# Kernel tuning notes

Measured on AMD Instinct MI355X. Metric: run time of the kernel, lower is better.

## Reference

```python
import jax, jax.numpy as jnp
import numpy as np

N = 100_000      # nodes
E = 3_200_000    # edges
F_IN = 9
F_HID = 9
F_OUT = 1
EPS = 1e-5

def _ln(x, g, b):
    m = x.mean(-1, keepdims=True)
    v = x.var(-1, keepdims=True)
    return (x - m) / jnp.sqrt(v + EPS) * g + b

def _gat(x, src, dst, edge_attr, W, a_src, a_dst, We, a_e, bias):
    # Single-head GATConv with edge_dim=1, add_self_loops=True, fill_value='mean'
    n = x.shape[0]
    loop = jnp.arange(n)
    deg = jax.ops.segment_sum(jnp.ones((src.shape[0],), x.dtype), dst, n)
    loop_attr = jax.ops.segment_sum(edge_attr, dst, n) / jnp.maximum(deg, 1.0)[:, None]
    s = jnp.concatenate([src, loop])
    d = jnp.concatenate([dst, loop])
    ea = jnp.concatenate([edge_attr, loop_attr], axis=0)   # [E+N, 1]
    xp = x @ W                                             # [N, C]
    a = (xp * a_src).sum(-1)[s] + (xp * a_dst).sum(-1)[d] + ((ea @ We) * a_e).sum(-1)
    a = jax.nn.leaky_relu(a, 0.2)
    amax = jax.ops.segment_max(a, d, n)
    aexp = jnp.exp(a - amax[d])
    denom = jax.ops.segment_sum(aexp, d, n)
    alpha = aexp / (denom[d] + 1e-16)
    return jax.ops.segment_sum(alpha[:, None] * xp[s], d, n) + bias

def setup_inputs() -> dict:
    key = jax.random.key(0)
    ks = jax.random.split(key, 16)
    def rn(k, shp, s):
        return jax.random.normal(k, shp, jnp.float32) * s
    return {
        "x": jax.random.normal(ks[0], (N, F_IN), jnp.float32),
        "edge_index": jax.random.randint(ks[1], (2, E), 0, N, jnp.int32),
        "edge_attr": jax.random.normal(ks[2], (E, 1), jnp.float32),
        "ln1_g": jnp.ones((F_IN,), jnp.float32), "ln1_b": jnp.zeros((F_IN,), jnp.float32),
        "W0": rn(ks[3], (F_IN, F_HID), 0.3), "as0": rn(ks[4], (F_HID,), 0.3),
        "ad0": rn(ks[5], (F_HID,), 0.3), "We0": rn(ks[6], (1, F_HID), 0.3),
        "ae0": rn(ks[7], (F_HID,), 0.3), "b0": jnp.zeros((F_HID,), jnp.float32),
        "W1": rn(ks[8], (F_HID, F_HID), 0.3), "as1": rn(ks[9], (F_HID,), 0.3),
        "ad1": rn(ks[10], (F_HID,), 0.3), "We1": rn(ks[11], (1, F_HID), 0.3),
        "ae1": rn(ks[12], (F_HID,), 0.3), "b1": jnp.zeros((F_HID,), jnp.float32),
        "ng1": jnp.ones((F_HID,), jnp.float32), "nb1": jnp.zeros((F_HID,), jnp.float32),
        "ln2_g": jnp.ones((2 * F_HID,), jnp.float32), "ln2_b": jnp.zeros((2 * F_HID,), jnp.float32),
        "et_W": rn(ks[13], (2 * F_HID, F_HID), 0.2), "et_b": jnp.zeros((F_HID,), jnp.float32),
        "fc_W": rn(ks[14], (F_HID, F_OUT), 0.3), "fc_b": jnp.zeros((F_OUT,), jnp.float32),
        "att_W": rn(ks[15], (2 * F_OUT, F_OUT), 0.5), "att_b": jnp.zeros((F_OUT,), jnp.float32),
    }

def reference(x, edge_index, edge_attr, ln1_g, ln1_b, W0, as0, ad0, We0, ae0, b0,
              W1, as1, ad1, We1, ae1, b1, ng1, nb1, ln2_g, ln2_b,
              et_W, et_b, fc_W, fc_b, att_W, att_b):
    src, dst = edge_index[0], edge_index[1]
    h = _ln(x, ln1_g, ln1_b)
    # layer 0: no norm/residual
    h = jax.nn.leaky_relu(_gat(h, src, dst, edge_attr, W0, as0, ad0, We0, ae0, b0), 0.01)
    # layer 1: norm + residual
    ident = h
    h = _ln(_gat(h, src, dst, edge_attr, W1, as1, ad1, We1, ae1, b1), ng1, nb1) + ident
    h = jax.nn.leaky_relu(h, 0.01)
    # edge path: gather-concat-norm-MLP  [E, 2H]
    ef = _ln(jnp.concatenate([h[src], h[dst]], axis=1), ln2_g, ln2_b)
    eo = jax.nn.leaky_relu(ef @ et_W + et_b, 0.01)
    eo = eo @ fc_W + fc_b                       # [E, 1]
    # AttentionLayer
    comb = jnp.concatenate([eo, edge_attr], axis=1)   # [E, 2]
    w = jax.nn.softmax(comb @ att_W + att_b, axis=-1) # [E, 1]
    att = (w * comb).sum(axis=1, keepdims=True)       # [E, 1]
    return att + eo
```

## Files before the change

### kernel.cpp

```cpp
#include <hip/hip_runtime.h>
#include <hip/hip_bf16.h>
#include <hip/hip_fp16.h>

typedef __hip_bfloat16 bf16;
typedef unsigned int uint;
typedef unsigned short ushort;
#define TPB 256
#define TPBS 512
#define TPBG 1024
#define BSH 7
#define BNODES 128
#define NBK_MAX 1024
#define CH 8192
#define EPT (CH / TPBS)
#define NW (TPBS / 64)
#define GPAD 16
#define CAP 4608

enum {
  LN1G = 0, LN1B = 9, PW0 = 18, AS0 = 99, AD0 = 108, CE0 = 117, B0 = 118,
  PW1 = 127, AS1 = 208, AD1 = 217, CE1 = 226, B1 = 227, NG = 236, NB = 245,
  LN2G = 254, LN2B = 272, ETW = 290, ETB = 452, FCW = 461, FCB = 470,
  GC = 471, KC = 480, ETH = 490, NPARAM = 580
};

#ifdef __has_builtin
#if __has_builtin(__builtin_amdgcn_fdot2)
#define HAVE_FDOT2 1
#endif
#endif
#ifndef HAVE_FDOT2
#define HAVE_FDOT2 0
#endif

typedef _Float16 h2f __attribute__((ext_vector_type(2)));

static __device__ __forceinline__ float lrelu(float x, float s) { return x >= 0.f ? x : s * x; }
static __device__ __forceinline__ float ldx(const void* p, long i, int isb) {
    return isb ? __bfloat162float(((const bf16*)p)[i]) : ((const float*)p)[i];
}
static __device__ __forceinline__ uint bfb(float f) {
    uint u = __float_as_uint(f);
    return (u + 0x7FFFu + ((u >> 16) & 1u)) >> 16;
}
static __device__ __forceinline__ uint pack2(float a, float b) { return bfb(a) | (bfb(b) << 16); }
static __device__ __forceinline__ float unlo(uint u) { return __uint_as_float(u << 16); }
static __device__ __forceinline__ float unhi(uint u) { return __uint_as_float(u & 0xFFFF0000u); }
static __device__ __forceinline__ ushort h16(float f) { return __half_as_ushort(__float2half(f)); }
static __device__ __forceinline__ uint p2h(float a, float b) { return (uint)h16(a) | ((uint)h16(b) << 16); }
static __device__ __forceinline__ float hfl(uint u) { return __half2float(__ushort_as_half((ushort)(u & 0xFFFFu))); }
static __device__ __forceinline__ float hfh(uint u) { return __half2float(__ushort_as_half((ushort)(u >> 16))); }
static __device__ __forceinline__ h2f as_h2(uint u) { union { uint u; h2f h; } x; x.u = u; return x.h; }
static __device__ __forceinline__ float dot2f(uint a, uint w, float acc) {
#if HAVE_FDOT2
    return __builtin_amdgcn_fdot2(as_h2(a), as_h2(w), acc, false);
#else
    return fmaf(hfl(a), hfl(w), fmaf(hfh(a), hfh(w), acc));
#endif
}

__global__ void k_params(const void* ln1g, const void* ln1b,
                         const void* W0, const void* as0, const void* ad0,
                         const void* We0, const void* ae0, const void* b0,
                         const void* W1, const void* as1, const void* ad1,
                         const void* We1, const void* ae1, const void* b1,
                         const void* ng, const void* nb,
                         const void* ln2g, const void* ln2b,
                         const void* etW, const void* etb,
                         const void* fcW, const void* fcb,
                         float* __restrict__ P, int* __restrict__ flagp,
                         int* __restrict__ gcursor, int nbk)
{
    __shared__ int sflag;
    if (threadIdx.x == 0) {
        unsigned short h0 = ((const unsigned short*)ln1g)[0];
        sflag = (h0 == 0x3F80u) ? 1 : 0;
        *flagp = sflag;
    }
    __syncthreads();
    const int f = sflag;
    const int t = threadIdx.x;
    for (int j = t; j < nbk; j += TPB) gcursor[j * GPAD] = j * CAP;
    for (int i = t; i < 9; i += TPB) {
        P[LN1G + i] = ldx(ln1g, i, f); P[LN1B + i] = ldx(ln1b, i, f);
        P[AS0 + i] = ldx(as0, i, f);   P[AD0 + i] = ldx(ad0, i, f);
        P[B0 + i]  = ldx(b0, i, f);
        P[AS1 + i] = ldx(as1, i, f);   P[AD1 + i] = ldx(ad1, i, f);
        P[B1 + i]  = ldx(b1, i, f);
        P[NG + i]  = ldx(ng, i, f);    P[NB + i]  = ldx(nb, i, f);
        P[ETB + i] = ldx(etb, i, f);   P[FCW + i] = ldx(fcW, i, f);
    }
    for (int i = t; i < 81; i += TPB) { P[PW0 + i] = ldx(W0, i, f); P[PW1 + i] = ldx(W1, i, f); }
    for (int i = t; i < 18; i += TPB) { P[LN2G + i] = ldx(ln2g, i, f); P[LN2B + i] = ldx(ln2b, i, f); }
    for (int i = t; i < 162; i += TPB) P[ETW + i] = ldx(etW, i, f) * ldx(ln2g, i / 9, f);
    __syncthreads();
    for (int i = t; i < 90; i += TPB) {
        int role = i / 45, rem = i % 45, c = rem / 5, p = rem % 5;
        int k0 = 2 * p, k1 = 2 * p + 1;
        float w0 = (k0 < 9) ? P[ETW + (role * 9 + k0) * 9 + c] : 0.f;
        float w1 = (k1 < 9) ? P[ETW + (role * 9 + k1) * 9 + c] : 0.f;
        ((uint*)P)[ETH + i] = p2h(w0, w1);
    }
    if (t == 0) {
        float c0 = 0.f, c1 = 0.f;
        for (int k = 0; k < 9; k++) {
            c0 += ldx(We0, k, f) * ldx(ae0, k, f);
            c1 += ldx(We1, k, f) * ldx(ae1, k, f);
        }
        P[CE0] = c0; P[CE1] = c1; P[FCB] = ldx(fcb, 0, f);
        for (int c = 0; c < 9; c++) {
            float gc = 0.f, kc = 0.f;
            for (int k = 0; k < 18; k++) {
                float wv = ldx(etW, (long)k * 9 + c, f);
                gc += ldx(ln2g, k, f) * wv;
                kc += ldx(ln2b, k, f) * wv;
            }
            P[GC + c] = gc;
            P[KC + c] = kc + ldx(etb, c, f);
        }
    }
}

__global__ void __launch_bounds__(TPBS)
k_bscatter(const int* __restrict__ src, const int* __restrict__ dst,
           const void* __restrict__ ea, const int* __restrict__ flagp,
           int* __restrict__ gcursor, int2* __restrict__ ebuf, int e, int nbk)
{
    __shared__ int cnt[NBK_MAX];
    __shared__ int cur[NBK_MAX];
    __shared__ int badj[NBK_MAX];
    __shared__ int wsum[NW];
    __shared__ int2 seb[CH];
    const int tid = threadIdx.x;
    const int lane = tid & 63;
    const int wid = tid >> 6;
    const int s0 = blockIdx.x * CH;
    const int m = min(e - s0, CH);
    const int fl = *flagp;
    cnt[tid] = 0; cnt[tid + TPBS] = 0;
    __syncthreads();
    int dreg[EPT]; int sreg[EPT]; float ereg[EPT];
    #pragma unroll
    for (int k = 0; k < EPT; k++) {
        int t = tid + k * TPBS;
        if (t < m) {
            dreg[k] = dst[s0 + t];
            sreg[k] = src[s0 + t];
            ereg[k] = ldx(ea, s0 + t, fl);
            atomicAdd(&cnt[dreg[k] >> BSH], 1);
        } else dreg[k] = -1;
    }
    __syncthreads();
    const int j0 = tid * 2, j1 = j0 + 1;
    int c0 = cnt[j0], c1 = cnt[j1];
    int lsum = c0 + c1;
    int sc = lsum;
    #pragma unroll
    for (int o = 1; o < 64; o <<= 1) {
        int v = __shfl_up(sc, o, 64);
        if (lane >= o) sc += v;
    }
    if (lane == 63) wsum[wid] = sc;
    __syncthreads();
    int woff = 0;
    #pragma unroll
    for (int w = 0; w < NW; w++) woff += (w < wid) ? wsum[w] : 0;
    int e0 = woff + sc - lsum;
    int e1 = e0 + c0;
    cur[j0] = e0; cur[j1] = e1;
    int gb0 = c0 ? atomicAdd(&gcursor[j0 * GPAD], c0) : 0;
    int gb1 = c1 ? atomicAdd(&gcursor[j1 * GPAD], c1) : 0;
    badj[j0] = gb0 - e0; badj[j1] = gb1 - e1;
    __syncthreads();
    #pragma unroll
    for (int k = 0; k < EPT; k++) {
        if (dreg[k] >= 0) {
            int d = dreg[k];
            int b = d >> BSH;
            int slot = atomicAdd(&cur[b], 1);
            seb[slot] = make_int2(sreg[k] | ((d & (BNODES - 1)) << 17),
                                  (int)(bfb(ereg[k]) | ((uint)b << 16)));
        }
    }
    __syncthreads();
    #pragma unroll
    for (int k = 0; k < EPT; k++) {
        int j = tid + k * TPBS;
        if (j < m) {
            int2 v = seb[j];
            int b = (int)((uint)v.y >> 16);
            int pos = badj[b] + j;
            if (pos < (b + 1) * CAP) {
                ebuf[pos] = make_int2(v.x, __float_as_int(unlo((uint)v.y)));
            }
        }
    }
}

__global__ void k_prep(const void* __restrict__ x, const float* __restrict__ P,
                       const int* __restrict__ flagp,
                       uint* __restrict__ xpb0, float* __restrict__ sd0, int n)
{
    const int fl = *flagp;
    int i = blockIdx.x * blockDim.x + threadIdx.x;
    if (i >= n) return;
    float h[9]; float m = 0.f;
    #pragma unroll
    for (int f = 0; f < 9; f++) { h[f] = ldx(x, (long)i * 9 + f, fl); m += h[f]; }
    m *= (1.f / 9.f);
    float v = 0.f;
    #pragma unroll
    for (int f = 0; f < 9; f++) { float d = h[f] - m; v += d * d; }
    float r = rsqrtf(v * (1.f / 9.f) + 1e-5f);
    #pragma unroll
    for (int f = 0; f < 9; f++) h[f] = (h[f] - m) * r * P[LN1G + f] + P[LN1B + f];
    float xr[9]; float ss = 0.f, sd = 0.f;
    #pragma unroll
    for (int c = 0; c < 9; c++) {
        float acc = 0.f;
        #pragma unroll
        for (int f = 0; f < 9; f++) acc += h[f] * P[PW0 + f * 9 + c];
        xr[c] = acc;
        ss += acc * P[AS0 + c]; sd += acc * P[AD0 + c];
    }
    uint* row = xpb0 + (size_t)i * 8;
    ((uint4*)row)[0] = make_uint4(pack2(xr[0], xr[1]), pack2(xr[2], xr[3]),
                                  pack2(xr[4], xr[5]), pack2(xr[6], xr[7]));
    ((uint4*)row)[1] = make_uint4(pack2(xr[8], ss), 0u, 0u, 0u);
    sd0[i] = sd;
}

__global__ void __launch_bounds__(TPBG)
k_sortg0(const int* __restrict__ gcursor, int2* __restrict__ ebuf,
         const float* __restrict__ P,
         const uint* __restrict__ xpb0, const float* __restrict__ sd0,
         float* __restrict__ h1, uint* __restrict__ xpb1,
         float* __restrict__ sd1, float* __restrict__ la,
         int* __restrict__ nodeoff, int n)
{
    __shared__ int2 seb[CAP];
    __shared__ ushort sidx[CAP];
    __shared__ int hist[BNODES], scn[BNODES], cur[BNODES];
    __shared__ int wtot[2];
    const int b = blockIdx.x, tid = threadIdx.x;
    const int beg = b * CAP;
    int cnt = gcursor[b * GPAD] - beg;
    if (cnt > CAP) cnt = CAP;
    if (cnt < 0) cnt = 0;
    if (tid < BNODES) hist[tid] = 0;
    __syncthreads();
    for (int j = tid; j < cnt; j += TPBG) {
        int2 v = ebuf[beg + j];
        seb[j] = v;
        atomicAdd(&hist[(v.x >> 17) & (BNODES - 1)], 1);
    }
    __syncthreads();
    int hc = 0, hsc = 0;
    if (tid < BNODES) {
        hc = hist[tid];
        hsc = hc;
        #pragma unroll
        for (int o = 1; o < 64; o <<= 1) {
            int v = __shfl_up(hsc, o, 64);
            if ((tid & 63) >= o) hsc += v;
        }
        if ((tid & 63) == 63) wtot[tid >> 6] = hsc;
    }
    __syncthreads();
    if (tid < BNODES) {
        int s2 = hsc + ((tid >= 64) ? wtot[0] : 0);
        scn[tid] = s2;
        cur[tid] = s2 - hc;
        nodeoff[b * BNODES + tid] = s2;
    }
    __syncthreads();
    for (int j = tid; j < cnt; j += TPBG) {
        int dl = (seb[j].x >> 17) & (BNODES - 1);
        int slot = atomicAdd(&cur[dl], 1);
        sidx[slot] = (ushort)j;
    }
    __syncthreads();
    for (int j = tid; j < cnt; j += TPBG) ebuf[beg + j] = seb[sidx[j]];
    const int nd = tid >> 3, l = tid & 7;
    const int i = (b << BSH) + nd;
    if (i < n) {
        const float ce = P[CE0];
        const int locend = scn[nd], locbeg = locend - hist[nd];
        const float sdi = sd0[i];
        float acc[11];
        #pragma unroll
        for (int k = 0; k < 11; k++) acc[k] = 0.f;
        for (int j = locbeg + l; j < locend; j += 8) {
            int2 sl = seb[sidx[j]];
            int s = sl.x & 0x1FFFF;
            float eav = __int_as_float(sl.y);
            const uint* row = xpb0 + (size_t)s * 8;
            uint4 q0 = *(const uint4*)row;
            uint  q2 = row[4];
            float ex = expf(lrelu(unhi(q2) + sdi + ce * eav, 0.2f));
            acc[0] += ex; acc[1] += eav;
            acc[2] += ex * unlo(q0.x); acc[3] += ex * unhi(q0.x);
            acc[4] += ex * unlo(q0.y); acc[5] += ex * unhi(q0.y);
            acc[6] += ex * unlo(q0.z); acc[7] += ex * unhi(q0.z);
            acc[8] += ex * unlo(q0.w); acc[9] += ex * unhi(q0.w);
            acc[10] += ex * unlo(q2);
        }
        #pragma unroll
        for (int k = 0; k < 11; k++) {
            acc[k] += __shfl_xor(acc[k], 1, 64);
            acc[k] += __shfl_xor(acc[k], 2, 64);
            acc[k] += __shfl_xor(acc[k], 4, 64);
        }
        if (l == 0) {
            float denom = acc[0];
            float S[9] = {acc[2], acc[3], acc[4], acc[5], acc[6], acc[7], acc[8], acc[9], acc[10]};
            float deg = (float)hist[nd];
            float lav = acc[1] / fmaxf(deg, 1.f);
            la[i] = lav;
            const uint* row = xpb0 + (size_t)i * 8;
            uint4 q0 = *(const uint4*)row;
            uint  q2 = row[4];
            float o0 = unlo(q0.x), o1 = unhi(q0.x), o2 = unlo(q0.y), o3 = unhi(q0.y);
            float o4 = unlo(q0.z), o5 = unhi(q0.z), o6 = unlo(q0.w), o7 = unhi(q0.w);
            float o8 = unlo(q2),   ssi = unhi(q2);
            float ex0 = expf(lrelu(ssi + sdi + ce * lav, 0.2f));
            denom += ex0;
            S[0] += ex0 * o0; S[1] += ex0 * o1; S[2] += ex0 * o2; S[3] += ex0 * o3;
            S[4] += ex0 * o4; S[5] += ex0 * o5; S[6] += ex0 * o6; S[7] += ex0 * o7;
            S[8] += ex0 * o8;
            float inv = 1.f / (denom + 1e-16f);
            float h[9];
            #pragma unroll
            for (int c = 0; c < 9; c++) h[c] = lrelu(S[c] * inv + P[B0 + c], 0.01f);
            float4* hr = (float4*)(h1 + (size_t)i * 12);
            hr[0] = make_float4(h[0], h[1], h[2], h[3]);
            hr[1] = make_float4(h[4], h[5], h[6], h[7]);
            hr[2] = make_float4(h[8], 0.f, 0.f, 0.f);
            float xr1[9]; float ss2 = 0.f, sd2 = 0.f;
            #pragma unroll
            for (int c = 0; c < 9; c++) {
                float a2 = 0.f;
                #pragma unroll
                for (int f = 0; f < 9; f++) a2 += h[f] * P[PW1 + f * 9 + c];
                xr1[c] = a2;
                ss2 += a2 * P[AS1 + c]; sd2 += a2 * P[AD1 + c];
            }
            uint* rw = xpb1 + (size_t)i * 8;
            ((uint4*)rw)[0] = make_uint4(pack2(xr1[0], xr1[1]), pack2(xr1[2], xr1[3]),
                                         pack2(xr1[4], xr1[5]), pack2(xr1[6], xr1[7]));
            ((uint4*)rw)[1] = make_uint4(pack2(xr1[8], ss2), 0u, 0u, 0u);
            sd1[i] = sd2;
        }
    }
}

__global__ void __launch_bounds__(TPBG)
k_sortg1(const int* __restrict__ nodeoff, const int2* __restrict__ ebuf,
         const float* __restrict__ P,
         const uint* __restrict__ xpb1, const float* __restrict__ sd1,
         const float* __restrict__ la, const float* __restrict__ h1,
         uint4* __restrict__ orec, int n)
{
    __shared__ int soff[BNODES];
    const int b = blockIdx.x, tid = threadIdx.x;
    const int beg = b * CAP;
    if (tid < BNODES) soff[tid] = nodeoff[b * BNODES + tid];
    __syncthreads();
    const int nd = tid >> 3, l = tid & 7;
    const int i = (b << BSH) + nd;
    if (i < n) {
        const float ce = P[CE1];
        const int locbeg = nd ? soff[nd - 1] : 0;
        const int locend = soff[nd];
        const float sdi = sd1[i];
        float acc[10];
        #pragma unroll
        for (int k = 0; k < 10; k++) acc[k] = 0.f;
        for (int j = locbeg + l; j < locend; j += 8) {
            int2 sl = ebuf[beg + j];
            int s = sl.x & 0x1FFFF;
            float eav = __int_as_float(sl.y);
            const uint* row = xpb1 + (size_t)s * 8;
            uint4 q0 = *(const uint4*)row;
            uint  q2 = row[4];
            float ex = expf(lrelu(unhi(q2) + sdi + ce * eav, 0.2f));
            acc[0] += ex;
            acc[1] += ex * unlo(q0.x); acc[2] += ex * unhi(q0.x);
            acc[3] += ex * unlo(q0.y); acc[4] += ex * unhi(q0.y);
            acc[5] += ex * unlo(q0.z); acc[6] += ex * unhi(q0.z);
            acc[7] += ex * unlo(q0.w); acc[8] += ex * unhi(q0.w);
            acc[9] += ex * unlo(q2);
        }
        #pragma unroll
        for (int k = 0; k < 10; k++) {
            acc[k] += __shfl_xor(acc[k], 1, 64);
            acc[k] += __shfl_xor(acc[k], 2, 64);
            acc[k] += __shfl_xor(acc[k], 4, 64);
        }
        if (l == 0) {
            float denom = acc[0];
            float S[9] = {acc[1], acc[2], acc[3], acc[4], acc[5], acc[6], acc[7], acc[8], acc[9]};
            const uint* row = xpb1 + (size_t)i * 8;
            uint4 q0 = *(const uint4*)row;
            uint  q2 = row[4];
            float o0 = unlo(q0.x), o1 = unhi(q0.x), o2 = unlo(q0.y), o3 = unhi(q0.y);
            float o4 = unlo(q0.z), o5 = unhi(q0.z), o6 = unlo(q0.w), o7 = unhi(q0.w);
            float o8 = unlo(q2),   ssi = unhi(q2);
            float ex0 = expf(lrelu(ssi + sdi + ce * la[i], 0.2f));
            denom += ex0;
            S[0] += ex0 * o0; S[1] += ex0 * o1; S[2] += ex0 * o2; S[3] += ex0 * o3;
            S[4] += ex0 * o4; S[5] += ex0 * o5; S[6] += ex0 * o6; S[7] += ex0 * o7;
            S[8] += ex0 * o8;
            float inv = 1.f / (denom + 1e-16f);
            float g[9]; float m = 0.f;
            #pragma unroll
            for (int c = 0; c < 9; c++) { g[c] = S[c] * inv + P[B1 + c]; m += g[c]; }
            m *= (1.f / 9.f);
            float v = 0.f;
            #pragma unroll
            for (int c = 0; c < 9; c++) { float d = g[c] - m; v += d * d; }
            float r = rsqrtf(v * (1.f / 9.f) + 1e-5f);
            const float4* hr = (const float4*)(h1 + (size_t)i * 12);
            float4 r0 = hr[0], r1 = hr[1], r2 = hr[2];
            float res[9] = {r0.x, r0.y, r0.z, r0.w, r1.x, r1.y, r1.z, r1.w, r2.x};
            float o[9];
            #pragma unroll
            for (int c = 0; c < 9; c++)
                o[c] = lrelu((g[c] - m) * r * P[NG + c] + P[NB + c] + res[c], 0.01f);
            float psum = 0.f, pss = 0.f;
            #pragma unroll
            for (int c = 0; c < 9; c++) { psum += o[c]; pss += o[c] * o[c]; }
            uint4* rp = orec + (size_t)i * 2;
            rp[0] = make_uint4(p2h(o[0], o[1]), p2h(o[2], o[3]), p2h(o[4], o[5]), p2h(o[6], o[7]));
            rp[1] = make_uint4(p2h(o[8], 0.f),
                               __float_as_uint(psum * (1.f / 18.f)),
                               __float_as_uint(pss * (1.f / 18.f)), 0u);
        }
    }
}

__global__ void __launch_bounds__(TPB)
k_edge(const int* __restrict__ src, const int* __restrict__ dst,
       const void* __restrict__ ea, const float* __restrict__ P,
       const int* __restrict__ flagp,
       const uint4* __restrict__ orec, void* __restrict__ outp, int e)
{
    const int fl = *flagp;
    const int base = blockIdx.x * (TPB * 2) + threadIdx.x;
    const uint* eth = (const uint*)P + ETH;
    #pragma unroll
    for (int q = 0; q < 2; q++) {
        int t = base + q * TPB;
        if (t < e) {
            int s = src[t], d = dst[t];
            const uint4* rs = orec + (size_t)s * 2;
            const uint4* rd = orec + (size_t)d * 2;
            uint4 As = rs[0], Bs = rs[1];
            uint4 Ad = rd[0], Bd = rd[1];
            float m   = __uint_as_float(Bs.y) + __uint_as_float(Bd.y);
            float ex2 = __uint_as_float(Bs.z) + __uint_as_float(Bd.z);
            float r = rsqrtf(fmaxf(ex2 - m * m, 0.f) + 1e-5f);
            float eo = P[FCB];
            #pragma unroll
            for (int c = 0; c < 9; c++) {
                float dotc = dot2f(As.x, eth[c * 5 + 0], 0.f);
                dotc = dot2f(As.y, eth[c * 5 + 1], dotc);
                dotc = dot2f(As.z, eth[c * 5 + 2], dotc);
                dotc = dot2f(As.w, eth[c * 5 + 3], dotc);
                dotc = dot2f(Bs.x, eth[c * 5 + 4], dotc);
                dotc = dot2f(Ad.x, eth[45 + c * 5 + 0], dotc);
                dotc = dot2f(Ad.y, eth[45 + c * 5 + 1], dotc);
                dotc = dot2f(Ad.z, eth[45 + c * 5 + 2], dotc);
                dotc = dot2f(Ad.w, eth[45 + c * 5 + 3], dotc);
                dotc = dot2f(Bd.x, eth[45 + c * 5 + 4], dotc);
                float pre = fmaf(r, fmaf(-m, P[GC + c], dotc), P[KC + c]);
                float act = fmaxf(pre, 0.01f * pre);
                eo = fmaf(act, P[FCW + c], eo);
            }
            float resv = 2.f * eo + ldx(ea, t, fl);
            if (fl) ((bf16*)outp)[t] = __float2bfloat16(resv);
            else    ((float*)outp)[t] = resv;
        }
    }
}

extern "C" void kernel_launch(void* const* d_in, const int* in_sizes, int n_in,
                              void* d_out, int out_size, void* d_ws, size_t ws_size,
                              hipStream_t stream) {
    const int n = in_sizes[0] / 9;
    const int e = in_sizes[2];
    const int nbk = (n + BNODES - 1) >> BSH;

    const void* X   = d_in[0];
    const int*  ei  = (const int*)d_in[1];
    const int*  src = ei;
    const int*  dst = ei + e;
    const void* EA  = d_in[2];

    char* base = (char*)d_ws;
    size_t off = 0;
    auto alloc = [&](size_t bytes) { void* p = base + off; off += (bytes + 63) & ~size_t(63); return p; };
    float*  P       = (float*)alloc(1024 * sizeof(float));
    int*    flagp   = (int*)(P + NPARAM);
    int*    gcursor = (int*)alloc((size_t)NBK_MAX * GPAD * sizeof(int));
    int2*   ebuf    = (int2*)alloc((size_t)nbk * CAP * sizeof(int2));
    uint*   xpb0    = (uint*)alloc((size_t)n * 8 * sizeof(uint));
    uint*   xpb1    = (uint*)alloc((size_t)n * 8 * sizeof(uint));
    float*  h1      = (float*)alloc((size_t)n * 12 * sizeof(float));
    uint4*  orec    = (uint4*)alloc((size_t)n * 2 * sizeof(uint4));
    int*    nodeoff = (int*)alloc((size_t)nbk * BNODES * sizeof(int));
    float*  sd0     = (float*)alloc((size_t)n * sizeof(float));
    float*  sd1     = (float*)alloc((size_t)n * sizeof(float));
    float*  la      = (float*)alloc((size_t)n * sizeof(float));

    dim3 gN((n + TPB - 1) / TPB);
    dim3 gE2((e + TPB * 2 - 1) / (TPB * 2));
    dim3 gC((e + CH - 1) / CH);
    dim3 gB(nbk);

    k_params<<<1, TPB, 0, stream>>>(d_in[3], d_in[4], d_in[5], d_in[6], d_in[7],
                                    d_in[8], d_in[9], d_in[10], d_in[11], d_in[12],
                                    d_in[13], d_in[14], d_in[15], d_in[16], d_in[17],
                                    d_in[18], d_in[19], d_in[20], d_in[21], d_in[22],
                                    d_in[23], d_in[24], P, flagp, gcursor, nbk);
    k_prep<<<gN, dim3(TPB), 0, stream>>>(X, P, flagp, xpb0, sd0, n);
    k_bscatter<<<gC, dim3(TPBS), 0, stream>>>(src, dst, EA, flagp, gcursor, ebuf, e, nbk);
    k_sortg0<<<gB, dim3(TPBG), 0, stream>>>(gcursor, ebuf, P, xpb0, sd0, h1, xpb1, sd1, la,
                                            nodeoff, n);
    k_sortg1<<<gB, dim3(TPBG), 0, stream>>>(nodeoff, ebuf, P, xpb1, sd1, la, h1, orec, n);
    k_edge<<<gE2, dim3(TPB), 0, stream>>>(src, dst, EA, P, flagp, orec, d_out, e);
}
```

Baseline: 182.2 us.

## Store sort permutation instead of rewriting edge buffer; widen bucket-scatter blocks

k_sortg0 no longer writes the sorted int2 edge records back to ebuf. It stores a 16-bit permutation index per edge instead, and k_sortg1 reloads the unsorted bucket plus that permutation into shared memory and walks edges through the indirection. This trades an 8-byte global write per edge for a 2-byte write plus an extra read and a larger shared-memory footprint in k_sortg1, which may lower occupancy. Separately, k_bscatter now uses 1024 threads, so each thread handles one bucket counter in the scan rather than two, and the count of edges per thread (EPT) drops.

```diff
diff --git a/kernel.cpp b/kernel.cpp
--- a/kernel.cpp
+++ b/kernel.cpp
@@ -6,7 +6,7 @@
 typedef unsigned int uint;
 typedef unsigned short ushort;
 #define TPB 256
-#define TPBS 512
+#define TPBS 1024
 #define TPBG 1024
 #define BSH 7
 #define BNODES 128
@@ -137,7 +137,7 @@
     const int s0 = blockIdx.x * CH;
     const int m = min(e - s0, CH);
     const int fl = *flagp;
-    cnt[tid] = 0; cnt[tid + TPBS] = 0;
+    cnt[tid] = 0;
     __syncthreads();
     int dreg[EPT]; int sreg[EPT]; float ereg[EPT];
     #pragma unroll
@@ -151,10 +151,8 @@
         } else dreg[k] = -1;
     }
     __syncthreads();
-    const int j0 = tid * 2, j1 = j0 + 1;
-    int c0 = cnt[j0], c1 = cnt[j1];
-    int lsum = c0 + c1;
-    int sc = lsum;
+    int c = cnt[tid];
+    int sc = c;
     #pragma unroll
     for (int o = 1; o < 64; o <<= 1) {
         int v = __shfl_up(sc, o, 64);
@@ -165,12 +163,10 @@
     int woff = 0;
     #pragma unroll
     for (int w = 0; w < NW; w++) woff += (w < wid) ? wsum[w] : 0;
-    int e0 = woff + sc - lsum;
-    int e1 = e0 + c0;
-    cur[j0] = e0; cur[j1] = e1;
-    int gb0 = c0 ? atomicAdd(&gcursor[j0 * GPAD], c0) : 0;
-    int gb1 = c1 ? atomicAdd(&gcursor[j1 * GPAD], c1) : 0;
-    badj[j0] = gb0 - e0; badj[j1] = gb1 - e1;
+    int ex = woff + sc - c;
+    cur[tid] = ex;
+    int gb = c ? atomicAdd(&gcursor[tid * GPAD], c) : 0;
+    badj[tid] = gb - ex;
     __syncthreads();
     #pragma unroll
     for (int k = 0; k < EPT; k++) {
@@ -231,12 +227,12 @@
 }
 
 __global__ void __launch_bounds__(TPBG)
-k_sortg0(const int* __restrict__ gcursor, int2* __restrict__ ebuf,
+k_sortg0(const int* __restrict__ gcursor, const int2* __restrict__ ebuf,
          const float* __restrict__ P,
          const uint* __restrict__ xpb0, const float* __restrict__ sd0,
          float* __restrict__ h1, uint* __restrict__ xpb1,
          float* __restrict__ sd1, float* __restrict__ la,
-         int* __restrict__ nodeoff, int n)
+         ushort* __restrict__ sidxg, int* __restrict__ nodeoff, int n)
 {
     __shared__ int2 seb[CAP];
     __shared__ ushort sidx[CAP];
@@ -280,7 +276,7 @@
         sidx[slot] = (ushort)j;
     }
     __syncthreads();
-    for (int j = tid; j < cnt; j += TPBG) ebuf[beg + j] = seb[sidx[j]];
+    for (int j = tid; j < cnt; j += TPBG) sidxg[beg + j] = sidx[j];
     const int nd = tid >> 3, l = tid & 7;
     const int i = (b << BSH) + nd;
     if (i < n) {
@@ -355,16 +351,24 @@
 }
 
 __global__ void __launch_bounds__(TPBG)
-k_sortg1(const int* __restrict__ nodeoff, const int2* __restrict__ ebuf,
-         const float* __restrict__ P,
+k_sortg1(const int* __restrict__ nodeoff, const ushort* __restrict__ sidxg,
+         const int2* __restrict__ ebuf, const float* __restrict__ P,
          const uint* __restrict__ xpb1, const float* __restrict__ sd1,
          const float* __restrict__ la, const float* __restrict__ h1,
          uint4* __restrict__ orec, int n)
 {
+    __shared__ int2 seb[CAP];
+    __shared__ ushort sidx[CAP];
     __shared__ int soff[BNODES];
     const int b = blockIdx.x, tid = threadIdx.x;
     const int beg = b * CAP;
     if (tid < BNODES) soff[tid] = nodeoff[b * BNODES + tid];
+    __syncthreads();
+    const int cnt = soff[BNODES - 1];
+    for (int j = tid; j < cnt; j += TPBG) {
+        seb[j] = ebuf[beg + j];
+        sidx[j] = sidxg[beg + j];
+    }
     __syncthreads();
     const int nd = tid >> 3, l = tid & 7;
     const int i = (b << BSH) + nd;
@@ -377,7 +381,7 @@
         #pragma unroll
         for (int k = 0; k < 10; k++) acc[k] = 0.f;
         for (int j = locbeg + l; j < locend; j += 8) {
-            int2 sl = ebuf[beg + j];
+            int2 sl = seb[sidx[j]];
             int s = sl.x & 0x1FFFF;
             float eav = __int_as_float(sl.y);
             const uint* row = xpb1 + (size_t)s * 8;
@@ -504,11 +508,12 @@
     int*    flagp   = (int*)(P + NPARAM);
     int*    gcursor = (int*)alloc((size_t)NBK_MAX * GPAD * sizeof(int));
     int2*   ebuf    = (int2*)alloc((size_t)nbk * CAP * sizeof(int2));
+    ushort* sidxg   = (ushort*)alloc((size_t)nbk * CAP * sizeof(ushort));
+    int*    nodeoff = (int*)alloc((size_t)nbk * BNODES * sizeof(int));
     uint*   xpb0    = (uint*)alloc((size_t)n * 8 * sizeof(uint));
     uint*   xpb1    = (uint*)alloc((size_t)n * 8 * sizeof(uint));
     float*  h1      = (float*)alloc((size_t)n * 12 * sizeof(float));
     uint4*  orec    = (uint4*)alloc((size_t)n * 2 * sizeof(uint4));
-    int*    nodeoff = (int*)alloc((size_t)nbk * BNODES * sizeof(int));
     float*  sd0     = (float*)alloc((size_t)n * sizeof(float));
     float*  sd1     = (float*)alloc((size_t)n * sizeof(float));
     float*  la      = (float*)alloc((size_t)n * sizeof(float));
@@ -526,7 +531,8 @@
     k_prep<<<gN, dim3(TPB), 0, stream>>>(X, P, flagp, xpb0, sd0, n);
     k_bscatter<<<gC, dim3(TPBS), 0, stream>>>(src, dst, EA, flagp, gcursor, ebuf, e, nbk);
     k_sortg0<<<gB, dim3(TPBG), 0, stream>>>(gcursor, ebuf, P, xpb0, sd0, h1, xpb1, sd1, la,
-                                            nodeoff, n);
-    k_sortg1<<<gB, dim3(TPBG), 0, stream>>>(nodeoff, ebuf, P, xpb1, sd1, la, h1, orec, n);
+                                            sidxg, nodeoff, n);
+    k_sortg1<<<gB, dim3(TPBG), 0, stream>>>(nodeoff, sidxg, ebuf, P, xpb1, sd1, la, h1,
+                                            orec, n);
     k_edge<<<gE2, dim3(TPB), 0, stream>>>(src, dst, EA, P, flagp, orec, d_out, e);
 }
```

After: 176.8 us. 3.0% less time.
